# Kernel optimization log

Measured on AMD Instinct MI355X. Metric: run time of the kernel, lower is better.

## Reference

```python
import jax, jax.numpy as jnp
import numpy as np

T, B, E, H = 1024, 4, 1024, 16
D = E // H  # head_dim = 64


def rel_shift(x):
    # Transformer-XL relative shift trick (RelativeShift.forward, batch_first=True).
    # x: [BH, Q, P] -> pad one zero column, reshape [BH, P+1, Q], drop first row, reshape back.
    BH, Q, P = x.shape
    zp = jnp.zeros((BH, Q, 1), x.dtype)
    xp = jnp.concatenate([zp, x], axis=2).reshape(BH, P + 1, Q)
    return xp[:, 1:, :].reshape(BH, Q, P)


def setup_inputs() -> dict:
    key = jax.random.key(0)
    ks = jax.random.split(key, 8)
    std = float(np.sqrt(2.0 / (E + E)))
    causal = jnp.triu(jnp.ones((T, T), dtype=bool), k=1)  # True = masked (future positions)
    return {
        "x": jax.random.normal(ks[0], (T, B, E), dtype=jnp.float32),
        "pos": jax.random.normal(ks[1], (T, 1, E), dtype=jnp.float32),
        "in_proj_weight": jax.random.normal(ks[2], (3 * E, E), dtype=jnp.float32) * std,
        "in_proj_bias": jnp.zeros((3 * E,), dtype=jnp.float32),
        "out_proj_weight": jax.random.normal(ks[3], (E, E), dtype=jnp.float32) * std,
        "out_proj_bias": jnp.zeros((E,), dtype=jnp.float32),
        "pos_proj_weight": jax.random.normal(ks[4], (E, E), dtype=jnp.float32) * std,
        "pos_proj_bias": jnp.zeros((E,), dtype=jnp.float32),
        "r_w_bias": jax.random.normal(ks[5], (H, D), dtype=jnp.float32) * 0.02,
        "r_r_bias": jax.random.normal(ks[6], (H, D), dtype=jnp.float32) * 0.02,
        "attn_mask": causal,
    }


def reference(x, pos, in_proj_weight, in_proj_bias, out_proj_weight, out_proj_bias,
              pos_proj_weight, pos_proj_bias, r_w_bias, r_r_bias, attn_mask):
    Tq, Bb, Ee = x.shape
    scale = 1.0 / np.sqrt(D).astype(np.float32)
    # fused QKV projection; layout [T, B, heads, 3, head_dim] matches
    # view(len_q, bsz*heads, 3, head_dim) in the original.
    qkv = (x @ in_proj_weight.T + in_proj_bias).reshape(Tq, Bb, H, 3, D)
    q = qkv[..., 0, :]  # [T,B,H,D]
    k = qkv[..., 1, :]
    v = qkv[..., 2, :]
    # position projection (shared across batch since pos is [T,1,E])
    r_head_k = (pos[:, 0, :] @ pos_proj_weight.T + pos_proj_bias).reshape(Tq, H, D)  # [P,H,D]
    rw_q = q + r_w_bias  # content bias
    rr_q = q + r_r_bias  # position bias
    ac = jnp.einsum('qbhd,kbhd->bhqk', rw_q, k) * scale            # [B,H,Q,K]
    bd = jnp.einsum('qbhd,phd->bhqp', rr_q, r_head_k) * scale      # [B,H,Q,P]
    bd = rel_shift(bd.reshape(Bb * H, Tq, Tq)).reshape(Bb, H, Tq, Tq)[..., :Tq]
    score = ac + bd
    score = jnp.where(attn_mask[None, None, :, :], -jnp.inf, score)
    attn = jax.nn.softmax(score, axis=-1)                          # [B,H,Q,K]
    ctx = jnp.einsum('bhqk,kbhd->qbhd', attn, v).reshape(Tq, Bb, Ee)
    out = ctx @ out_proj_weight.T + out_proj_bias                  # [T,B,E]
    return out, attn
```

## Files before the change

kernel.cpp:

```cpp
#include <hip/hip_runtime.h>
#include <math.h>

#define TQ 1024
#define BBATCH 4
#define EDIM 1024
#define HHEADS 16
#define DHEAD 64

typedef __bf16 bf16x8 __attribute__((ext_vector_type(8)));
typedef __bf16 bf16x4 __attribute__((ext_vector_type(4)));
typedef float  f32x4  __attribute__((ext_vector_type(4)));

__device__ __forceinline__ bf16x8 cvt8(float4 a, float4 b) {
    bf16x8 w;
    w[0]=(__bf16)a.x; w[1]=(__bf16)a.y; w[2]=(__bf16)a.z; w[3]=(__bf16)a.w;
    w[4]=(__bf16)b.x; w[5]=(__bf16)b.y; w[6]=(__bf16)b.z; w[7]=(__bf16)b.w;
    return w;
}

#define LDK 40

__device__ __forceinline__ void gemm_body(
    const float* __restrict__ A, const float* __restrict__ B,
    const float* __restrict__ bias, float* __restrict__ C,
    int N, int K, int m0, int n0, int mode,
    __bf16* As, __bf16* Bs)
{
    const int tid  = threadIdx.x;
    const int lane = tid & 63;
    const int wid  = tid >> 6;
    const int wr   = wid >> 1, wc = wid & 1;

    f32x4 accf[4][4] = {};

    const int sm0 = tid >> 2;
    const int sm1 = sm0 + 64;
    const int sk  = (tid & 3) << 3;

    const int fr = lane & 15;
    const int kg = (lane >> 4) << 3;

    for (int k0 = 0; k0 < K; k0 += 32) {
        float4 ra0a = *(const float4*)&A[(size_t)(m0 + sm0) * K + k0 + sk];
        float4 ra0b = *(const float4*)&A[(size_t)(m0 + sm0) * K + k0 + sk + 4];
        float4 ra1a = *(const float4*)&A[(size_t)(m0 + sm1) * K + k0 + sk];
        float4 ra1b = *(const float4*)&A[(size_t)(m0 + sm1) * K + k0 + sk + 4];
        float4 rb0a = *(const float4*)&B[(size_t)(n0 + sm0) * K + k0 + sk];
        float4 rb0b = *(const float4*)&B[(size_t)(n0 + sm0) * K + k0 + sk + 4];
        float4 rb1a = *(const float4*)&B[(size_t)(n0 + sm1) * K + k0 + sk];
        float4 rb1b = *(const float4*)&B[(size_t)(n0 + sm1) * K + k0 + sk + 4];

        __syncthreads();

        *(bf16x8*)&As[sm0 * LDK + sk] = cvt8(ra0a, ra0b);
        *(bf16x8*)&As[sm1 * LDK + sk] = cvt8(ra1a, ra1b);
        *(bf16x8*)&Bs[sm0 * LDK + sk] = cvt8(rb0a, rb0b);
        *(bf16x8*)&Bs[sm1 * LDK + sk] = cvt8(rb1a, rb1b);

        __syncthreads();

        bf16x8 af[4], bfr[4];
        #pragma unroll
        for (int i = 0; i < 4; ++i) {
            af[i]  = *(const bf16x8*)&As[(wr * 64 + i * 16 + fr) * LDK + kg];
            bfr[i] = *(const bf16x8*)&Bs[(wc * 64 + i * 16 + fr) * LDK + kg];
        }
        #pragma unroll
        for (int mi = 0; mi < 4; ++mi)
        #pragma unroll
        for (int ni = 0; ni < 4; ++ni)
            accf[mi][ni] = __builtin_amdgcn_mfma_f32_16x16x32_bf16(
                af[mi], bfr[ni], accf[mi][ni], 0, 0, 0);
    }

    const int fq = lane >> 4;
    #pragma unroll
    for (int mi = 0; mi < 4; ++mi)
    #pragma unroll
    for (int ni = 0; ni < 4; ++ni) {
        int row = m0 + wr * 64 + mi * 16 + fq * 4;
        int col = n0 + wc * 64 + ni * 16 + fr;
        float bv = bias[col];
        #pragma unroll
        for (int j = 0; j < 4; ++j) {
            float v = accf[mi][ni][j] + bv;
            if (mode == 0) {
                C[(size_t)(row + j) * N + col] = v;
            } else {
                C[(((size_t)(col >> 6) << 10) + (row + j)) * 64 + (col & 63)] = v;
            }
        }
    }
}

__global__ __launch_bounds__(256) void gemm_dual_kernel(
    const float* __restrict__ x, const float* __restrict__ w_in,
    const float* __restrict__ b_in, float* __restrict__ qkv,
    const float* __restrict__ pos, const float* __restrict__ w_pos,
    const float* __restrict__ b_pos, float* __restrict__ Rm)
{
    __shared__ __bf16 As[128 * LDK];
    __shared__ __bf16 Bs[128 * LDK];
    if (blockIdx.y < 32) {
        gemm_body(x, w_in, b_in, qkv, 3072, 1024,
                  blockIdx.y * 128, blockIdx.x * 128, 0, As, Bs);
    } else {
        if (blockIdx.x >= 8) return;
        gemm_body(pos, w_pos, b_pos, Rm, 1024, 1024,
                  (blockIdx.y - 32) * 128, blockIdx.x * 128, 1, As, Bs);
    }
}

__global__ __launch_bounds__(256) void gemm_out_kernel(
    const float* __restrict__ A, const float* __restrict__ B,
    const float* __restrict__ bias, float* __restrict__ C)
{
    __shared__ __bf16 As[128 * LDK];
    __shared__ __bf16 Bs[128 * LDK];
    gemm_body(A, B, bias, C, 1024, 1024,
              blockIdx.y * 128, blockIdx.x * 128, 0, As, Bs);
}

__global__ __launch_bounds__(256) void bias_dots_kernel(
    const float* __restrict__ qkv, const float* __restrict__ Rm,
    const float* __restrict__ rwb, const float* __restrict__ rrb,
    float* __restrict__ cK, float* __restrict__ cR)
{
    int id = blockIdx.x * 256 + threadIdx.x;
    if (id < 65536) {
        int bh = id >> 10, k = id & 1023;
        int b = bh >> 4, h = bh & 15;
        const float* p = &qkv[((size_t)k * 4 + b) * 3072 + h * 192 + 64];
        const float* w = &rwb[h << 6];
        float s = 0.f;
        #pragma unroll
        for (int d = 0; d < 64; d += 4) {
            float4 v = *(const float4*)&p[d];
            s += v.x * w[d] + v.y * w[d + 1] + v.z * w[d + 2] + v.w * w[d + 3];
        }
        cK[id] = s;
    } else if (id < 81920) {
        int id2 = id - 65536;
        int h = id2 >> 10, j = id2 & 1023;
        const float* p = &Rm[(((size_t)h << 10) + j) * 64];
        const float* w = &rrb[h << 6];
        float s = 0.f;
        #pragma unroll
        for (int d = 0; d < 64; d += 4) {
            float4 v = *(const float4*)&p[d];
            s += v.x * w[d] + v.y * w[d + 1] + v.z * w[d + 2] + v.w * w[d + 3];
        }
        cR[id2] = s;
    }
}

#define SLD 72

__global__ __launch_bounds__(256) void score_tile_kernel(
    const float* __restrict__ qkv, const float* __restrict__ Rm,
    const float* __restrict__ cK, const float* __restrict__ cR,
    float* __restrict__ attn, float2* __restrict__ part)
{
    int t = blockIdx.x;
    int qt = (int)((sqrtf(8.f * t + 1.f) - 1.f) * 0.5f);
    while ((qt + 1) * (qt + 2) / 2 <= t) ++qt;
    while (qt * (qt + 1) / 2 > t) --qt;
    int kt = t - qt * (qt + 1) / 2;

    const int bh = blockIdx.y;
    const int b = bh >> 4, h = bh & 15;
    const int q0 = qt << 6, k0 = kt << 6;
    const int tid = threadIdx.x, lane = tid & 63, wid = tid >> 6;
    const int fr = lane & 15, fq = lane >> 4, kg = fq << 3;
    const int w16 = wid << 4;
    const int base_j = k0 - q0 + 960;

    __shared__ __align__(16) char smem[36864];
    __bf16* Qs = (__bf16*)smem;
    __bf16* Ks = (__bf16*)(smem + 9216);
    __bf16* R0 = (__bf16*)(smem + 18432);
    __bf16* R1 = (__bf16*)(smem + 27648);
    float (*BDs)[68] = (float(*)[68])smem;

    float4 qreg[4], kreg[4], r0reg[4], r1reg[4];
    #pragma unroll
    for (int s = 0; s < 4; ++s) {
        int idx = (s << 8) + tid;
        int r = idx >> 4, dc = (idx & 15) << 2;
        qreg[s] = *(const float4*)&qkv[((size_t)(q0 + r) * 4 + b) * 3072 + h * 192 + dc];
        kreg[s] = *(const float4*)&qkv[((size_t)(k0 + r) * 4 + b) * 3072 + h * 192 + 64 + dc];
        int j0 = base_j + r;       if (j0 > 1023) j0 = 1023;
        int j1 = base_j + 64 + r;  if (j1 > 1023) j1 = 1023;
        r0reg[s] = *(const float4*)&Rm[(((size_t)h << 10) + j0) * 64 + dc];
        r1reg[s] = *(const float4*)&Rm[(((size_t)h << 10) + j1) * 64 + dc];
    }
    #pragma unroll
    for (int s = 0; s < 4; ++s) {
        int idx = (s << 8) + tid;
        int r = idx >> 4, dc = (idx & 15) << 2;
        bf16x4 w;
        w[0]=(__bf16)qreg[s].x; w[1]=(__bf16)qreg[s].y; w[2]=(__bf16)qreg[s].z; w[3]=(__bf16)qreg[s].w;
        *(bf16x4*)&Qs[r * SLD + dc] = w;
        w[0]=(__bf16)kreg[s].x; w[1]=(__bf16)kreg[s].y; w[2]=(__bf16)kreg[s].z; w[3]=(__bf16)kreg[s].w;
        *(bf16x4*)&Ks[r * SLD + dc] = w;
        w[0]=(__bf16)r0reg[s].x; w[1]=(__bf16)r0reg[s].y; w[2]=(__bf16)r0reg[s].z; w[3]=(__bf16)r0reg[s].w;
        *(bf16x4*)&R0[r * SLD + dc] = w;
        w[0]=(__bf16)r1reg[s].x; w[1]=(__bf16)r1reg[s].y; w[2]=(__bf16)r1reg[s].z; w[3]=(__bf16)r1reg[s].w;
        *(bf16x4*)&R1[r * SLD + dc] = w;
    }
    __syncthreads();

    bf16x8 af0 = *(const bf16x8*)&Qs[(w16 + fr) * SLD + kg];
    bf16x8 af1 = *(const bf16x8*)&Qs[(w16 + fr) * SLD + 32 + kg];

    f32x4 aac[4], abd[4];
    const f32x4 z4 = {0.f, 0.f, 0.f, 0.f};

    #pragma unroll
    for (int ni = 0; ni < 4; ++ni) {
        bf16x8 b0 = *(const bf16x8*)&Ks[(ni * 16 + fr) * SLD + kg];
        bf16x8 b1 = *(const bf16x8*)&Ks[(ni * 16 + fr) * SLD + 32 + kg];
        aac[ni] = __builtin_amdgcn_mfma_f32_16x16x32_bf16(af0, b0, z4, 0, 0, 0);
        aac[ni] = __builtin_amdgcn_mfma_f32_16x16x32_bf16(af1, b1, aac[ni], 0, 0, 0);
    }
    #pragma unroll
    for (int ni = 0; ni < 4; ++ni) {
        bf16x8 b0 = *(const bf16x8*)&R0[(ni * 16 + fr) * SLD + kg];
        bf16x8 b1 = *(const bf16x8*)&R0[(ni * 16 + fr) * SLD + 32 + kg];
        abd[ni] = __builtin_amdgcn_mfma_f32_16x16x32_bf16(af0, b0, z4, 0, 0, 0);
        abd[ni] = __builtin_amdgcn_mfma_f32_16x16x32_bf16(af1, b1, abd[ni], 0, 0, 0);
    }

    __syncthreads();

    #pragma unroll
    for (int ni = 0; ni < 4; ++ni)
    #pragma unroll
    for (int j = 0; j < 4; ++j)
        BDs[w16 + fq * 4 + j][ni * 16 + fr] = abd[ni][j];
    asm volatile("s_waitcnt lgkmcnt(0)" ::: "memory");
    #pragma unroll
    for (int ni = 0; ni < 4; ++ni)
    #pragma unroll
    for (int j = 0; j < 4; ++j) {
        int lrow = w16 + fq * 4 + j;
        int widx = (ni * 16 + fr) - lrow + 63;
        if (widx < 64) aac[ni][j] += BDs[lrow][widx];
    }
    asm volatile("s_waitcnt lgkmcnt(0)" ::: "memory");

    #pragma unroll
    for (int ni = 0; ni < 4; ++ni) {
        bf16x8 b0 = *(const bf16x8*)&R1[(ni * 16 + fr) * SLD + kg];
        bf16x8 b1 = *(const bf16x8*)&R1[(ni * 16 + fr) * SLD + 32 + kg];
        abd[ni] = __builtin_amdgcn_mfma_f32_16x16x32_bf16(af0, b0, z4, 0, 0, 0);
        abd[ni] = __builtin_amdgcn_mfma_f32_16x16x32_bf16(af1, b1, abd[ni], 0, 0, 0);
    }
    #pragma unroll
    for (int ni = 0; ni < 4; ++ni)
    #pragma unroll
    for (int j = 0; j < 4; ++j)
        BDs[w16 + fq * 4 + j][ni * 16 + fr] = abd[ni][j];
    asm volatile("s_waitcnt lgkmcnt(0)" ::: "memory");
    #pragma unroll
    for (int ni = 0; ni < 4; ++ni)
    #pragma unroll
    for (int j = 0; j < 4; ++j) {
        int lrow = w16 + fq * 4 + j;
        int widx = (ni * 16 + fr) - lrow + 63;
        if (widx >= 64) aac[ni][j] += BDs[lrow][widx - 64];
    }

    float sc[4][4];
    #pragma unroll
    for (int ni = 0; ni < 4; ++ni) {
        int lcol = ni * 16 + fr;
        int k = k0 + lcol;
        float ckv = cK[(bh << 10) + k];
        #pragma unroll
        for (int j = 0; j < 4; ++j) {
            int lrow = w16 + fq * 4 + j;
            int q = q0 + lrow;
            int widx = lcol - lrow + 63;
            int jidx = base_j + widx; if (jidx > 1023) jidx = 1023;
            float crv = cR[(h << 10) + jidx];
            float v = 0.125f * (aac[ni][j] + ckv + crv);
            if (kt == qt && lcol > lrow) v = -1e30f;
            sc[ni][j] = v;
            attn[((((size_t)bh << 10) + q) << 10) + k] = v;
        }
    }
    #pragma unroll
    for (int j = 0; j < 4; ++j) {
        float tmax = fmaxf(fmaxf(sc[0][j], sc[1][j]), fmaxf(sc[2][j], sc[3][j]));
        tmax = fmaxf(tmax, __shfl_xor(tmax, 1));
        tmax = fmaxf(tmax, __shfl_xor(tmax, 2));
        tmax = fmaxf(tmax, __shfl_xor(tmax, 4));
        tmax = fmaxf(tmax, __shfl_xor(tmax, 8));
        float ps = __expf(sc[0][j] - tmax) + __expf(sc[1][j] - tmax)
                 + __expf(sc[2][j] - tmax) + __expf(sc[3][j] - tmax);
        ps += __shfl_xor(ps, 1); ps += __shfl_xor(ps, 2);
        ps += __shfl_xor(ps, 4); ps += __shfl_xor(ps, 8);
        if (fr == 0)
            part[(((size_t)(bh << 10) + q0 + w16 + fq * 4 + j) << 4) + kt]
                = make_float2(tmax, ps);
    }
}

__global__ __launch_bounds__(256) void stats_reduce_kernel(
    const float2* __restrict__ part, float2* __restrict__ stats,
    float* __restrict__ ctx)
{
    const int row = blockIdx.x * 256 + threadIdx.x;
    const int q = row & 1023;
    const int nt = (q >> 6) + 1;
    float2 pr[16];
    float m = -1e30f;
    for (int kt = 0; kt < nt; ++kt) {
        pr[kt] = part[((size_t)row << 4) + kt];
        m = fmaxf(m, pr[kt].x);
    }
    float s = 0.f;
    for (int kt = 0; kt < nt; ++kt)
        s += pr[kt].y * __expf(pr[kt].x - m);
    stats[row] = make_float2(m, 1.0f / s);

    const float4 z = {0.f, 0.f, 0.f, 0.f};
    #pragma unroll
    for (int i = 0; i < 16; ++i)
        *(float4*)&ctx[((size_t)i * 65536 + row) * 4] = z;
}

#define FLD 66

__global__ __launch_bounds__(256) void ctx_split_kernel(
    const float* __restrict__ qkv, const float2* __restrict__ stats,
    float* __restrict__ attn, float* __restrict__ ctx)
{
    const int pid = blockIdx.x;
    const int qt = 15 - (pid >> 1);
    const int half = pid & 1;
    const int n = qt + 1;
    const int nh0 = (n + 1) >> 1;
    const int kts = half ? nh0 : 0;
    const int kte = half ? n : nh0;

    const int bh = blockIdx.y;
    const int b = bh >> 4, h = bh & 15;
    const int q0 = qt << 6;
    const int tid = threadIdx.x, lane = tid & 63, wid = tid >> 6;
    const int fr = lane & 15, fq = lane >> 4, kg = fq << 3;
    const int w16 = wid << 4;
    const int c4 = (tid & 15) << 2;
    const int rb = tid >> 4;

    __shared__ __bf16 Pl[64 * FLD];
    __shared__ __bf16 Vt[64 * FLD];

    float mrow[4], inv[4];
    #pragma unroll
    for (int s = 0; s < 4; ++s) {
        float2 st = stats[(bh << 10) + q0 + rb + (s << 4)];
        mrow[s] = st.x; inv[s] = st.y;
    }

    f32x4 apv[4] = {};
    float4 vcur[4], pcur[4];
    if (kte > kts) {
        const int k0 = kts << 6;
        #pragma unroll
        for (int s = 0; s < 4; ++s) {
            int r = rb + (s << 4);
            vcur[s] = *(const float4*)&qkv[((size_t)(k0 + r) * 4 + b) * 3072 + h * 192 + 128 + c4];
            pcur[s] = *(const float4*)&attn[((size_t)bh << 20) + ((size_t)(q0 + r) << 10) + k0 + c4];
        }
    }

    for (int kt = kts; kt < kte; ++kt) {
        const int k0 = kt << 6;
        __syncthreads();
        #pragma unroll
        for (int s = 0; s < 4; ++s) {
            int r = rb + (s << 4);
            Vt[(c4 + 0) * FLD + r] = (__bf16)vcur[s].x;
            Vt[(c4 + 1) * FLD + r] = (__bf16)vcur[s].y;
            Vt[(c4 + 2) * FLD + r] = (__bf16)vcur[s].z;
            Vt[(c4 + 3) * FLD + r] = (__bf16)vcur[s].w;
            float4 p;
            p.x = __expf(pcur[s].x - mrow[s]) * inv[s];
            p.y = __expf(pcur[s].y - mrow[s]) * inv[s];
            p.z = __expf(pcur[s].z - mrow[s]) * inv[s];
            p.w = __expf(pcur[s].w - mrow[s]) * inv[s];
            *(float4*)&attn[((size_t)bh << 20) + ((size_t)(q0 + r) << 10) + k0 + c4] = p;
            bf16x4 pw;
            pw[0]=(__bf16)p.x; pw[1]=(__bf16)p.y; pw[2]=(__bf16)p.z; pw[3]=(__bf16)p.w;
            *(bf16x4*)&Pl[r * FLD + c4] = pw;
        }
        float4 vnxt[4], pnxt[4];
        if (kt + 1 < kte) {
            const int k1 = (kt + 1) << 6;
            #pragma unroll
            for (int s = 0; s < 4; ++s) {
                int r = rb + (s << 4);
                vnxt[s] = *(const float4*)&qkv[((size_t)(k1 + r) * 4 + b) * 3072 + h * 192 + 128 + c4];
                pnxt[s] = *(const float4*)&attn[((size_t)bh << 20) + ((size_t)(q0 + r) << 10) + k1 + c4];
            }
        }
        __syncthreads();
        bf16x8 pa0 = *(const bf16x8*)&Pl[(w16 + fr) * FLD + kg];
        bf16x8 pa1 = *(const bf16x8*)&Pl[(w16 + fr) * FLD + 32 + kg];
        #pragma unroll
        for (int ni = 0; ni < 4; ++ni) {
            bf16x8 bv0 = *(const bf16x8*)&Vt[(ni * 16 + fr) * FLD + kg];
            bf16x8 bv1 = *(const bf16x8*)&Vt[(ni * 16 + fr) * FLD + 32 + kg];
            apv[ni] = __builtin_amdgcn_mfma_f32_16x16x32_bf16(pa0, bv0, apv[ni], 0, 0, 0);
            apv[ni] = __builtin_amdgcn_mfma_f32_16x16x32_bf16(pa1, bv1, apv[ni], 0, 0, 0);
        }
        if (kt + 1 < kte) {
            #pragma unroll
            for (int s = 0; s < 4; ++s) { vcur[s] = vnxt[s]; pcur[s] = pnxt[s]; }
        }
    }

    if (half) {
        for (int kt = n; kt < 16; ++kt) {
            const int k0 = kt << 6;
            #pragma unroll
            for (int s = 0; s < 4; ++s) {
                int r = rb + (s << 4);
                float4 z = {0.f, 0.f, 0.f, 0.f};
                *(float4*)&attn[((size_t)bh << 20) + ((size_t)(q0 + r) << 10) + k0 + c4] = z;
            }
        }
    }

    if (kte > kts) {
        #pragma unroll
        for (int ni = 0; ni < 4; ++ni)
        #pragma unroll
        for (int j = 0; j < 4; ++j)
            atomicAdd(&ctx[((size_t)(q0 + w16 + fq * 4 + j) * 4 + b) * 1024
                           + (h << 6) + ni * 16 + fr], apv[ni][j]);
    }
}

extern "C" void kernel_launch(void* const* d_in, const int* in_sizes, int n_in,
                              void* d_out, int out_size, void* d_ws, size_t ws_size,
                              hipStream_t stream)
{
    (void)in_sizes; (void)n_in; (void)out_size; (void)ws_size;
    const float* x     = (const float*)d_in[0];
    const float* pos   = (const float*)d_in[1];
    const float* w_in  = (const float*)d_in[2];
    const float* b_in  = (const float*)d_in[3];
    const float* w_out = (const float*)d_in[4];
    const float* b_out = (const float*)d_in[5];
    const float* w_pos = (const float*)d_in[6];
    const float* b_pos = (const float*)d_in[7];
    const float* rwb   = (const float*)d_in[8];
    const float* rrb   = (const float*)d_in[9];

    float* out  = (float*)d_out;
    float* attn = out + (size_t)TQ * BBATCH * EDIM;

    float* ws  = (float*)d_ws;
    float* qkv = ws;
    float* R   = qkv + (size_t)4096 * 3072;
    float* ctx = R + (size_t)HHEADS * TQ * DHEAD;
    float*  cK    = out;
    float*  cR    = out + 65536;
    float2* stats = (float2*)(out + 81920);
    float2* part  = (float2*)(out + 262144);

    dim3 blk(256, 1, 1);

    gemm_dual_kernel<<<dim3(24, 40), blk, 0, stream>>>(
        x, w_in, b_in, qkv, pos, w_pos, b_pos, R);
    bias_dots_kernel<<<dim3(320), blk, 0, stream>>>(qkv, R, rwb, rrb, cK, cR);
    score_tile_kernel<<<dim3(136, 64), blk, 0, stream>>>(qkv, R, cK, cR, attn, part);
    stats_reduce_kernel<<<dim3(256), blk, 0, stream>>>(part, stats, ctx);
    ctx_split_kernel<<<dim3(32, 64), blk, 0, stream>>>(qkv, stats, attn, ctx);
    gemm_out_kernel<<<dim3(8, 32), blk, 0, stream>>>(ctx, w_out, b_out, out);
}
```

Baseline: 370.2 us.

## Fold stats reduction into ctx kernel and split ctx into two halves

Removes the separate stats_reduce kernel: each ctx_split block now recomputes row max and sum from the per-tile partials. When the workspace is large enough, ctx is written to two separate buffers (one per half split) with plain stores instead of atomics, and the output GEMM adds the two buffers while loading A. The score kernel stages cK/cR values in shared memory, and attn stores become nontemporal. This trades a kernel launch, a ctx zeroing pass and atomics for redundant stats computation and an extra read stream in the output GEMM.

```diff
diff --git a/kernel.cpp b/kernel.cpp
--- a/kernel.cpp
+++ b/kernel.cpp
@@ -17,11 +17,20 @@
     w[4]=(__bf16)b.x; w[5]=(__bf16)b.y; w[6]=(__bf16)b.z; w[7]=(__bf16)b.w;
     return w;
 }
+__device__ __forceinline__ float4 add4(float4 a, float4 b) {
+    return make_float4(a.x + b.x, a.y + b.y, a.z + b.z, a.w + b.w);
+}
+__device__ __forceinline__ void nt_store4(float x, float y, float z, float w,
+                                          float* dst) {
+    f32x4 v; v[0] = x; v[1] = y; v[2] = z; v[3] = w;
+    __builtin_nontemporal_store(v, (f32x4*)dst);
+}
 
 #define LDK 40
 
 __device__ __forceinline__ void gemm_body(
-    const float* __restrict__ A, const float* __restrict__ B,
+    const float* __restrict__ A, const float* __restrict__ A2,
+    const float* __restrict__ B,
     const float* __restrict__ bias, float* __restrict__ C,
     int N, int K, int m0, int n0, int mode,
     __bf16* As, __bf16* Bs)
@@ -45,6 +54,12 @@
         float4 ra0b = *(const float4*)&A[(size_t)(m0 + sm0) * K + k0 + sk + 4];
         float4 ra1a = *(const float4*)&A[(size_t)(m0 + sm1) * K + k0 + sk];
         float4 ra1b = *(const float4*)&A[(size_t)(m0 + sm1) * K + k0 + sk + 4];
+        if (A2) {
+            ra0a = add4(ra0a, *(const float4*)&A2[(size_t)(m0 + sm0) * K + k0 + sk]);
+            ra0b = add4(ra0b, *(const float4*)&A2[(size_t)(m0 + sm0) * K + k0 + sk + 4]);
+            ra1a = add4(ra1a, *(const float4*)&A2[(size_t)(m0 + sm1) * K + k0 + sk]);
+            ra1b = add4(ra1b, *(const float4*)&A2[(size_t)(m0 + sm1) * K + k0 + sk + 4]);
+        }
         float4 rb0a = *(const float4*)&B[(size_t)(n0 + sm0) * K + k0 + sk];
         float4 rb0b = *(const float4*)&B[(size_t)(n0 + sm0) * K + k0 + sk + 4];
         float4 rb1a = *(const float4*)&B[(size_t)(n0 + sm1) * K + k0 + sk];
@@ -102,22 +117,23 @@
     __shared__ __bf16 As[128 * LDK];
     __shared__ __bf16 Bs[128 * LDK];
     if (blockIdx.y < 32) {
-        gemm_body(x, w_in, b_in, qkv, 3072, 1024,
+        gemm_body(x, nullptr, w_in, b_in, qkv, 3072, 1024,
                   blockIdx.y * 128, blockIdx.x * 128, 0, As, Bs);
     } else {
         if (blockIdx.x >= 8) return;
-        gemm_body(pos, w_pos, b_pos, Rm, 1024, 1024,
+        gemm_body(pos, nullptr, w_pos, b_pos, Rm, 1024, 1024,
                   (blockIdx.y - 32) * 128, blockIdx.x * 128, 1, As, Bs);
     }
 }
 
 __global__ __launch_bounds__(256) void gemm_out_kernel(
-    const float* __restrict__ A, const float* __restrict__ B,
+    const float* __restrict__ A, const float* __restrict__ A2,
+    const float* __restrict__ B,
     const float* __restrict__ bias, float* __restrict__ C)
 {
     __shared__ __bf16 As[128 * LDK];
     __shared__ __bf16 Bs[128 * LDK];
-    gemm_body(A, B, bias, C, 1024, 1024,
+    gemm_body(A, A2, B, bias, C, 1024, 1024,
               blockIdx.y * 128, blockIdx.x * 128, 0, As, Bs);
 }
 
@@ -175,12 +191,22 @@
     const int w16 = wid << 4;
     const int base_j = k0 - q0 + 960;
 
-    __shared__ __align__(16) char smem[36864];
+    __shared__ __align__(16) char smem[37888];
     __bf16* Qs = (__bf16*)smem;
     __bf16* Ks = (__bf16*)(smem + 9216);
     __bf16* R0 = (__bf16*)(smem + 18432);
     __bf16* R1 = (__bf16*)(smem + 27648);
+    float* cKs = (float*)(smem + 36864);
+    float* cRs = (float*)(smem + 36864 + 256);
     float (*BDs)[68] = (float(*)[68])smem;
+
+    if (tid < 64) {
+        cKs[tid] = cK[(bh << 10) + k0 + tid];
+    } else if (tid < 191) {
+        int i = tid - 64;
+        int j = base_j + i; if (j > 1023) j = 1023;
+        cRs[i] = cR[(h << 10) + j];
+    }
 
     float4 qreg[4], kreg[4], r0reg[4], r1reg[4];
     #pragma unroll
@@ -276,15 +302,13 @@
     for (int ni = 0; ni < 4; ++ni) {
         int lcol = ni * 16 + fr;
         int k = k0 + lcol;
-        float ckv = cK[(bh << 10) + k];
+        float ckv = cKs[lcol];
         #pragma unroll
         for (int j = 0; j < 4; ++j) {
             int lrow = w16 + fq * 4 + j;
             int q = q0 + lrow;
             int widx = lcol - lrow + 63;
-            int jidx = base_j + widx; if (jidx > 1023) jidx = 1023;
-            float crv = cR[(h << 10) + jidx];
-            float v = 0.125f * (aac[ni][j] + ckv + crv);
+            float v = 0.125f * (aac[ni][j] + ckv + cRs[widx]);
             if (kt == qt && lcol > lrow) v = -1e30f;
             sc[ni][j] = v;
             attn[((((size_t)bh << 10) + q) << 10) + k] = v;
@@ -307,35 +331,13 @@
     }
 }
 
-__global__ __launch_bounds__(256) void stats_reduce_kernel(
-    const float2* __restrict__ part, float2* __restrict__ stats,
-    float* __restrict__ ctx)
-{
-    const int row = blockIdx.x * 256 + threadIdx.x;
-    const int q = row & 1023;
-    const int nt = (q >> 6) + 1;
-    float2 pr[16];
-    float m = -1e30f;
-    for (int kt = 0; kt < nt; ++kt) {
-        pr[kt] = part[((size_t)row << 4) + kt];
-        m = fmaxf(m, pr[kt].x);
-    }
-    float s = 0.f;
-    for (int kt = 0; kt < nt; ++kt)
-        s += pr[kt].y * __expf(pr[kt].x - m);
-    stats[row] = make_float2(m, 1.0f / s);
-
-    const float4 z = {0.f, 0.f, 0.f, 0.f};
-    #pragma unroll
-    for (int i = 0; i < 16; ++i)
-        *(float4*)&ctx[((size_t)i * 65536 + row) * 4] = z;
-}
-
 #define FLD 66
 
+template<int MODE>
 __global__ __launch_bounds__(256) void ctx_split_kernel(
-    const float* __restrict__ qkv, const float2* __restrict__ stats,
-    float* __restrict__ attn, float* __restrict__ ctx)
+    const float* __restrict__ qkv, const float2* __restrict__ part,
+    float* __restrict__ attn, float* __restrict__ ctx0,
+    float* __restrict__ ctx1)
 {
     const int pid = blockIdx.x;
     const int qt = 15 - (pid >> 1);
@@ -360,8 +362,13 @@
     float mrow[4], inv[4];
     #pragma unroll
     for (int s = 0; s < 4; ++s) {
-        float2 st = stats[(bh << 10) + q0 + rb + (s << 4)];
-        mrow[s] = st.x; inv[s] = st.y;
+        const int row = (bh << 10) + q0 + rb + (s << 4);
+        const float2* pp = &part[(size_t)row << 4];
+        float m = -1e30f;
+        for (int kt = 0; kt <= qt; ++kt) m = fmaxf(m, pp[kt].x);
+        float sum = 0.f;
+        for (int kt = 0; kt <= qt; ++kt) sum += pp[kt].y * __expf(pp[kt].x - m);
+        mrow[s] = m; inv[s] = 1.0f / sum;
     }
 
     f32x4 apv[4] = {};
@@ -386,14 +393,14 @@
             Vt[(c4 + 1) * FLD + r] = (__bf16)vcur[s].y;
             Vt[(c4 + 2) * FLD + r] = (__bf16)vcur[s].z;
             Vt[(c4 + 3) * FLD + r] = (__bf16)vcur[s].w;
-            float4 p;
-            p.x = __expf(pcur[s].x - mrow[s]) * inv[s];
-            p.y = __expf(pcur[s].y - mrow[s]) * inv[s];
-            p.z = __expf(pcur[s].z - mrow[s]) * inv[s];
-            p.w = __expf(pcur[s].w - mrow[s]) * inv[s];
-            *(float4*)&attn[((size_t)bh << 20) + ((size_t)(q0 + r) << 10) + k0 + c4] = p;
+            float px = __expf(pcur[s].x - mrow[s]) * inv[s];
+            float py = __expf(pcur[s].y - mrow[s]) * inv[s];
+            float pz = __expf(pcur[s].z - mrow[s]) * inv[s];
+            float pw4 = __expf(pcur[s].w - mrow[s]) * inv[s];
+            nt_store4(px, py, pz, pw4,
+                &attn[((size_t)bh << 20) + ((size_t)(q0 + r) << 10) + k0 + c4]);
             bf16x4 pw;
-            pw[0]=(__bf16)p.x; pw[1]=(__bf16)p.y; pw[2]=(__bf16)p.z; pw[3]=(__bf16)p.w;
+            pw[0]=(__bf16)px; pw[1]=(__bf16)py; pw[2]=(__bf16)pz; pw[3]=(__bf16)pw4;
             *(bf16x4*)&Pl[r * FLD + c4] = pw;
         }
         float4 vnxt[4], pnxt[4];
@@ -428,19 +435,29 @@
             #pragma unroll
             for (int s = 0; s < 4; ++s) {
                 int r = rb + (s << 4);
-                float4 z = {0.f, 0.f, 0.f, 0.f};
-                *(float4*)&attn[((size_t)bh << 20) + ((size_t)(q0 + r) << 10) + k0 + c4] = z;
+                nt_store4(0.f, 0.f, 0.f, 0.f,
+                    &attn[((size_t)bh << 20) + ((size_t)(q0 + r) << 10) + k0 + c4]);
             }
         }
     }
 
-    if (kte > kts) {
+    if (MODE == 0) {
+        float* ctxH = half ? ctx1 : ctx0;
         #pragma unroll
         for (int ni = 0; ni < 4; ++ni)
         #pragma unroll
         for (int j = 0; j < 4; ++j)
-            atomicAdd(&ctx[((size_t)(q0 + w16 + fq * 4 + j) * 4 + b) * 1024
-                           + (h << 6) + ni * 16 + fr], apv[ni][j]);
+            ctxH[((size_t)(q0 + w16 + fq * 4 + j) * 4 + b) * 1024
+                 + (h << 6) + ni * 16 + fr] = apv[ni][j];
+    } else {
+        if (kte > kts) {
+            #pragma unroll
+            for (int ni = 0; ni < 4; ++ni)
+            #pragma unroll
+            for (int j = 0; j < 4; ++j)
+                atomicAdd(&ctx0[((size_t)(q0 + w16 + fq * 4 + j) * 4 + b) * 1024
+                                + (h << 6) + ni * 16 + fr], apv[ni][j]);
+        }
     }
 }
 
@@ -448,7 +465,7 @@
                               void* d_out, int out_size, void* d_ws, size_t ws_size,
                               hipStream_t stream)
 {
-    (void)in_sizes; (void)n_in; (void)out_size; (void)ws_size;
+    (void)in_sizes; (void)n_in; (void)out_size;
     const float* x     = (const float*)d_in[0];
     const float* pos   = (const float*)d_in[1];
     const float* w_in  = (const float*)d_in[2];
@@ -463,13 +480,15 @@
     float* out  = (float*)d_out;
     float* attn = out + (size_t)TQ * BBATCH * EDIM;
 
-    float* ws  = (float*)d_ws;
-    float* qkv = ws;
-    float* R   = qkv + (size_t)4096 * 3072;
-    float* ctx = R + (size_t)HHEADS * TQ * DHEAD;
+    float* ws   = (float*)d_ws;
+    float* qkv  = ws;
+    float* R    = qkv + (size_t)4096 * 3072;
+    float* ctx0 = R + (size_t)HHEADS * TQ * DHEAD;
+    float* ctx1 = ctx0 + (size_t)TQ * BBATCH * EDIM;
+    const size_t need_dual = (size_t)(ctx1 + (size_t)TQ * BBATCH * EDIM - ws) * 4;
+    const bool dual = ws_size >= need_dual;
     float*  cK    = out;
     float*  cR    = out + 65536;
-    float2* stats = (float2*)(out + 81920);
     float2* part  = (float2*)(out + 262144);
 
     dim3 blk(256, 1, 1);
@@ -478,7 +497,16 @@
         x, w_in, b_in, qkv, pos, w_pos, b_pos, R);
     bias_dots_kernel<<<dim3(320), blk, 0, stream>>>(qkv, R, rwb, rrb, cK, cR);
     score_tile_kernel<<<dim3(136, 64), blk, 0, stream>>>(qkv, R, cK, cR, attn, part);
-    stats_reduce_kernel<<<dim3(256), blk, 0, stream>>>(part, stats, ctx);
-    ctx_split_kernel<<<dim3(32, 64), blk, 0, stream>>>(qkv, stats, attn, ctx);
-    gemm_out_kernel<<<dim3(8, 32), blk, 0, stream>>>(ctx, w_out, b_out, out);
-}
+    if (dual) {
+        ctx_split_kernel<0><<<dim3(32, 64), blk, 0, stream>>>(
+            qkv, part, attn, ctx0, ctx1);
+        gemm_out_kernel<<<dim3(8, 32), blk, 0, stream>>>(ctx0, ctx1, w_out, b_out, out);
+    } else {
+        hipError_t _e = hipMemsetAsync(ctx0, 0,
+            (size_t)TQ * BBATCH * EDIM * sizeof(float), stream);
+        (void)_e;
+        ctx_split_kernel<1><<<dim3(32, 64), blk, 0, stream>>>(
+            qkv, part, attn, ctx0, nullptr);
+        gemm_out_kernel<<<dim3(8, 32), blk, 0, stream>>>(ctx0, nullptr, w_out, b_out, out);
+    }
+}
```

New measurement: 380.0 us. 1.03x slower.
